# Performance work log

Hardware: AMD Instinct MI355X
Metric: run time of the kernel (lower is better)

## Reference

```python
import jax, jax.numpy as jnp
import numpy as np
from jax import lax

REPR, ACT, HID = 256, 2, 512
BN_EPS = 1e-5


def setup_inputs() -> dict:
    key = jax.random.key(0)
    ks = jax.random.split(key, 12)
    B, H, W, Tm1 = 512, 64, 64, 16
    d_in = REPR + ACT
    s = lambda k, shape, scale: jax.random.normal(k, shape, dtype=jnp.float32) * scale
    return {
        "init_state": jax.random.normal(ks[0], (B, 2, H, W), dtype=jnp.float32),
        "actions": jax.random.normal(ks[1], (B, Tm1, ACT), dtype=jnp.float32),
        "conv_w": s(ks[2], (16, 2, 3, 3), (1.0 / np.sqrt(2 * 9))),
        "bn_gamma": jnp.ones((16,), jnp.float32),
        "bn_beta": jnp.zeros((16,), jnp.float32),
        "enc_fc_w": s(ks[3], (REPR, 16), (1.0 / np.sqrt(16))),
        "enc_fc_b": s(ks[4], (REPR,), 0.01),
        "gru_w_ih": s(ks[5], (3 * HID, d_in), (1.0 / np.sqrt(HID))),
        "gru_w_hh": s(ks[6], (3 * HID, HID), (1.0 / np.sqrt(HID))),
        "gru_b_ih": s(ks[7], (3 * HID,), (1.0 / np.sqrt(HID))),
        "gru_b_hh": s(ks[8], (3 * HID,), (1.0 / np.sqrt(HID))),
        "pred_fc_w": s(ks[9], (REPR, HID), (1.0 / np.sqrt(HID))),
        "pred_fc_b": s(ks[10], (REPR,), 0.01),
    }


def _encoder(x, conv_w, bn_gamma, bn_beta, enc_fc_w, enc_fc_b):
    # Conv2d(2->16, 3x3, stride 1, pad 1, no bias), NCHW
    y = lax.conv_general_dilated(x, conv_w, (1, 1), "SAME",
                                 dimension_numbers=("NCHW", "OIHW", "NCHW"))
    # BatchNorm2d in training mode: batch statistics over (N, H, W)
    mean = jnp.mean(y, axis=(0, 2, 3), keepdims=True)
    var = jnp.var(y, axis=(0, 2, 3), keepdims=True)
    y = (y - mean) * lax.rsqrt(var + BN_EPS)
    y = y * bn_gamma[None, :, None, None] + bn_beta[None, :, None, None]
    y = jax.nn.relu(y)
    # MaxPool2d(2, 2)
    y = lax.reduce_window(y, -jnp.inf, lax.max, (1, 1, 2, 2), (1, 1, 2, 2), "VALID")
    # AdaptiveAvgPool2d((1,1)) + flatten
    y = jnp.mean(y, axis=(2, 3))  # (B, 16)
    return y @ enc_fc_w.T + enc_fc_b  # (B, repr_dim)


def reference(init_state, actions, conv_w, bn_gamma, bn_beta, enc_fc_w, enc_fc_b,
              gru_w_ih, gru_w_hh, gru_b_ih, gru_b_hh, pred_fc_w, pred_fc_b):
    B = init_state.shape[0]
    s0 = _encoder(init_state, conv_w, bn_gamma, bn_beta, enc_fc_w, enc_fc_b)  # (B, R)

    def step(carry, u_t):
        s_prev, h = carry
        x = jnp.concatenate([s_prev, u_t], axis=-1)          # (B, R+A)
        gx = x @ gru_w_ih.T + gru_b_ih                        # (B, 3H)
        gh = h @ gru_w_hh.T + gru_b_hh                        # (B, 3H)
        gx_r, gx_z, gx_n = jnp.split(gx, 3, axis=-1)
        gh_r, gh_z, gh_n = jnp.split(gh, 3, axis=-1)
        r = jax.nn.sigmoid(gx_r + gh_r)
        z = jax.nn.sigmoid(gx_z + gh_z)
        n = jnp.tanh(gx_n + r * gh_n)
        h_new = (1.0 - z) * n + z * h
        s_pred = jax.nn.relu(h_new @ pred_fc_w.T + pred_fc_b)  # (B, R)
        return (s_pred, h_new), s_pred

    h0 = jnp.zeros((B, HID), dtype=s0.dtype)
    u_seq = jnp.transpose(actions, (1, 0, 2))  # (T-1, B, A)
    _, preds = lax.scan(step, (s0, h0), u_seq)  # preds: (T-1, B, R)
    pred_encs = jnp.concatenate([s0[None], preds], axis=0)  # (T, B, R)
    return jnp.transpose(pred_encs, (1, 0, 2))  # (B, T, R)
```

## Files before the change

kernel.cpp:

```cpp
#include <hip/hip_runtime.h>
#include <hip/hip_bf16.h>
#include <math.h>

#define TM1 16
#define TT 17

typedef __attribute__((ext_vector_type(8))) __bf16 bf16x8;
typedef __attribute__((ext_vector_type(4))) float f32x4;

#define OFF_BSTATS 0
#define OFF_STATS  65536
#define OFF_POOLED 65568
#define OFF_BCOL   98336
#define OFF_SPB    104480
#define OFF_PWB    170016
#define OFF_WIHB   235552
#define OFF_WHHB   432160
#define OFF_HB     825376

#define IMG_STRIDE 67
#define SLAB_ROWS 18
#define IMG_CI (SLAB_ROWS * IMG_STRIDE)

__device__ __forceinline__ void stage_slab_bf16(__hip_bfloat16* __restrict__ imgp,
                                                const float* __restrict__ xb, int slab,
                                                int tid) {
  for (int i = tid; i < 2 * SLAB_ROWS * 66; i += 256) {
    const int ci = i / (SLAB_ROWS * 66);
    const int rem = i - ci * (SLAB_ROWS * 66);
    const int lr = rem / 66, c = rem - lr * 66;
    const int gr = slab * 16 - 1 + lr;
    float v = 0.0f;
    if (gr >= 0 && gr < 64 && c >= 1 && c <= 64) v = xb[ci * 4096 + gr * 64 + (c - 1)];
    imgp[ci * IMG_CI + lr * IMG_STRIDE + c] = __float2bfloat16(v);
  }
}

__device__ __forceinline__ void make_k_offsets(int hi, int* off, int* val) {
#pragma unroll
  for (int j = 0; j < 8; ++j) {
    const int k = hi * 8 + j;
    if (k < 18) {
      const int ci = k / 9, r9 = k - ci * 9;
      const int dy = r9 / 3, dx = r9 - dy * 3;
      off[j] = ci * IMG_CI + dy * IMG_STRIDE + dx;
      val[j] = 1;
    } else {
      off[j] = 0;
      val[j] = 0;
    }
  }
}

__device__ __forceinline__ bf16x8 make_conv_bfrag(const float* __restrict__ cw,
                                                  int l15, int hi) {
  __hip_bfloat16 btmp[8];
#pragma unroll
  for (int j = 0; j < 8; ++j) {
    const int k = hi * 8 + j;
    btmp[j] = __float2bfloat16((k < 18) ? cw[l15 * 18 + k] : 0.0f);
  }
  return *(bf16x8*)btmp;
}

__device__ __forceinline__ bf16x8 make_conv_afrag(const __hip_bfloat16* __restrict__ imgp,
                                                  int yloc, int x0, int l15,
                                                  const int* off, const int* val) {
  const int base = yloc * IMG_STRIDE + x0 + l15;
  const __hip_bfloat16 z = __float2bfloat16(0.0f);
  __hip_bfloat16 atmp[8];
#pragma unroll
  for (int j = 0; j < 8; ++j) atmp[j] = val[j] ? imgp[base + off[j]] : z;
  return *(bf16x8*)atmp;
}

__global__ __launch_bounds__(256) void enc_stats_prep(
    const float* __restrict__ x, const float* __restrict__ cw,
    float* __restrict__ bstats,
    const float* __restrict__ wih, const float* __restrict__ whh,
    const float* __restrict__ pw,
    const float* __restrict__ bih, const float* __restrict__ bhh,
    __hip_bfloat16* __restrict__ wihb, __hip_bfloat16* __restrict__ whhb,
    __hip_bfloat16* __restrict__ pwb, float* __restrict__ bcol) {
  {
    const int n1 = 1536 * 256, n2 = 1536 * 512, n3 = 256 * 512, n4 = 512 * 12;
    int i = blockIdx.x * 256 + threadIdx.x;
    int st = gridDim.x * 256;
    for (int j = i; j < n1 + n2 + n3 + n4; j += st) {
      if (j < n1) {
        int r = j >> 8, c = j & 255;
        wihb[j] = __float2bfloat16(wih[r * 258 + c]);
      } else if (j < n1 + n2) {
        int k = j - n1;
        whhb[k] = __float2bfloat16(whh[k]);
      } else if (j < n1 + n2 + n3) {
        int k = j - n1 - n2;
        pwb[k] = __float2bfloat16(pw[k]);
      } else {
        int k = j - n1 - n2 - n3;
        int col = k / 12, e = k - col * 12;
        float v = 0.0f;
        switch (e) {
          case 0: v = bih[col] + bhh[col]; break;
          case 1: v = bih[512 + col] + bhh[512 + col]; break;
          case 2: v = bih[1024 + col]; break;
          case 3: v = bhh[1024 + col]; break;
          case 4: v = wih[col * 258 + 256]; break;
          case 5: v = wih[col * 258 + 257]; break;
          case 6: v = wih[(512 + col) * 258 + 256]; break;
          case 7: v = wih[(512 + col) * 258 + 257]; break;
          case 8: v = wih[(1024 + col) * 258 + 256]; break;
          case 9: v = wih[(1024 + col) * 258 + 257]; break;
          default: v = 0.0f; break;
        }
        bcol[k] = v;
      }
    }
  }

  __shared__ __hip_bfloat16 imgp[2 * IMG_CI];
  __shared__ float redS[4][16], redQ[4][16];
  const int tid = threadIdx.x;
  const int b = blockIdx.x >> 2, slab = blockIdx.x & 3;
  const int wv = tid >> 6, lane = tid & 63;
  const int l15 = lane & 15, hi = lane >> 4;
  stage_slab_bf16(imgp, x + b * 8192, slab, tid);

  int off[8], val[8];
  make_k_offsets(hi, off, val);
  const bf16x8 bfrag = make_conv_bfrag(cw, l15, hi);
  __syncthreads();

  float sacc = 0.0f, qacc = 0.0f;
  const f32x4 zero4 = {0.f, 0.f, 0.f, 0.f};
#pragma unroll
  for (int tp = 0; tp < 8; ++tp) {
    const int tpi = wv * 8 + tp;
    const int y0 = (tpi >> 2) * 2, x0 = (tpi & 3) * 16;
    bf16x8 a0 = make_conv_afrag(imgp, y0, x0, l15, off, val);
    bf16x8 a1 = make_conv_afrag(imgp, y0 + 1, x0, l15, off, val);
    f32x4 c0 = __builtin_amdgcn_mfma_f32_16x16x32_bf16(a0, bfrag, zero4, 0, 0, 0);
    f32x4 c1 = __builtin_amdgcn_mfma_f32_16x16x32_bf16(a1, bfrag, zero4, 0, 0, 0);
#pragma unroll
    for (int i = 0; i < 4; ++i) {
      sacc += c0[i] + c1[i];
      qacc = fmaf(c0[i], c0[i], qacc);
      qacc = fmaf(c1[i], c1[i], qacc);
    }
  }
  sacc += __shfl_down(sacc, 16); sacc += __shfl_down(sacc, 32);
  qacc += __shfl_down(qacc, 16); qacc += __shfl_down(qacc, 32);
  if (lane < 16) { redS[wv][l15] = sacc; redQ[wv][l15] = qacc; }
  __syncthreads();
  if (tid < 16)
    bstats[tid * 2048 + blockIdx.x] =
        redS[0][tid] + redS[1][tid] + redS[2][tid] + redS[3][tid];
  else if (tid < 32) {
    int c = tid - 16;
    bstats[tid * 2048 + blockIdx.x] =
        redQ[0][c] + redQ[1][c] + redQ[2][c] + redQ[3][c];
  }
}

__global__ __launch_bounds__(256) void reduce_stats_k(const float* __restrict__ bstats,
                                                      float* __restrict__ stats) {
  __shared__ float acc[4];
  const int c = blockIdx.x, tid = threadIdx.x;
  const float4 v4 = *(const float4*)(bstats + c * 2048 + tid * 8);
  const float4 w4 = *(const float4*)(bstats + c * 2048 + tid * 8 + 4);
  float v = v4.x + v4.y + v4.z + v4.w + w4.x + w4.y + w4.z + w4.w;
#pragma unroll
  for (int off = 32; off >= 1; off >>= 1) v += __shfl_down(v, off);
  if ((tid & 63) == 0) acc[tid >> 6] = v;
  __syncthreads();
  if (tid == 0) stats[c] = acc[0] + acc[1] + acc[2] + acc[3];
}

__global__ __launch_bounds__(256) void enc_pool(const float* __restrict__ x,
                                                const float* __restrict__ cw,
                                                const float* __restrict__ stats,
                                                const float* __restrict__ gamma,
                                                const float* __restrict__ beta,
                                                float* __restrict__ pooledG) {
  __shared__ __hip_bfloat16 imgp[2 * IMG_CI];
  __shared__ float red[4][16];
  __shared__ float statsL[32];
  const int tid = threadIdx.x;
  const int b = blockIdx.x >> 2, slab = blockIdx.x & 3;
  const int wv = tid >> 6, lane = tid & 63;
  const int l15 = lane & 15, hi = lane >> 4;
  stage_slab_bf16(imgp, x + b * 8192, slab, tid);
  if (tid < 32) statsL[tid] = stats[tid];

  int off[8], val[8];
  make_k_offsets(hi, off, val);
  const bf16x8 bfrag = make_conv_bfrag(cw, l15, hi);
  __syncthreads();

  const float invN = 1.0f / (512.0f * 4096.0f);
  const float m = statsL[l15] * invN;
  const float var = statsL[16 + l15] * invN - m * m;
  const float isd = rsqrtf(var + 1e-5f);
  const float scv = gamma[l15] * isd;
  const float shv = beta[l15] - m * scv;

  float psum = 0.0f;
  const f32x4 zero4 = {0.f, 0.f, 0.f, 0.f};
#pragma unroll
  for (int tp = 0; tp < 8; ++tp) {
    const int tpi = wv * 8 + tp;
    const int y0 = (tpi >> 2) * 2, x0 = (tpi & 3) * 16;
    bf16x8 a0 = make_conv_afrag(imgp, y0, x0, l15, off, val);
    bf16x8 a1 = make_conv_afrag(imgp, y0 + 1, x0, l15, off, val);
    f32x4 c0 = __builtin_amdgcn_mfma_f32_16x16x32_bf16(a0, bfrag, zero4, 0, 0, 0);
    f32x4 c1 = __builtin_amdgcn_mfma_f32_16x16x32_bf16(a1, bfrag, zero4, 0, 0, 0);
#pragma unroll
    for (int p = 0; p < 2; ++p) {
      const float v00 = fmaxf(fmaf(c0[2 * p + 0], scv, shv), 0.0f);
      const float v01 = fmaxf(fmaf(c0[2 * p + 1], scv, shv), 0.0f);
      const float v10 = fmaxf(fmaf(c1[2 * p + 0], scv, shv), 0.0f);
      const float v11 = fmaxf(fmaf(c1[2 * p + 1], scv, shv), 0.0f);
      psum += fmaxf(fmaxf(v00, v01), fmaxf(v10, v11));
    }
  }
  psum += __shfl_down(psum, 16);
  psum += __shfl_down(psum, 32);
  if (lane < 16) red[wv][l15] = psum;
  __syncthreads();
  if (tid < 16)
    pooledG[blockIdx.x * 16 + tid] = red[0][tid] + red[1][tid] + red[2][tid] + red[3][tid];
}

__global__ __launch_bounds__(384) void gru_v2(
    const __hip_bfloat16* __restrict__ spb,
    const __hip_bfloat16* __restrict__ hb_in,
    __hip_bfloat16* __restrict__ hb_out,
    const __hip_bfloat16* __restrict__ wihb,
    const __hip_bfloat16* __restrict__ whhb,
    const float* __restrict__ bcol,
    const float* __restrict__ actions,
    const float* __restrict__ pooledG,
    const float* __restrict__ fcw,
    const float* __restrict__ fcb,
    float* __restrict__ out,
    int t) {
  __shared__ __hip_bfloat16 sF[8 * 64 * 8];
  __shared__ __hip_bfloat16 hF[16 * 64 * 8];
  __shared__ float accL[4][2][256];
  const int tid = threadIdx.x;
  const int w = tid / 64, lane = tid & 63;
  const int l15 = lane & 15, hi = lane >> 4;
  const int cg = blockIdx.x, band = blockIdx.y;
  const int row0 = band * 16;
  const int ct = w & 1, g = w >> 1;

  if (t == 0) {
    float* avgF = &accL[0][0][0];
    if (tid < 256) {
      const int r = tid >> 4, k = tid & 15;
      const int img = row0 + r;
      const float v = pooledG[(img * 4 + 0) * 16 + k] + pooledG[(img * 4 + 1) * 16 + k] +
                      pooledG[(img * 4 + 2) * 16 + k] + pooledG[(img * 4 + 3) * 16 + k];
      avgF[r * 16 + k] = v * (1.0f / 1024.0f);
    }
    __syncthreads();
    for (int i = tid; i < 4096; i += 384) {
      const int kk = i >> 9, rem = i & 511, ln = rem >> 3, e = rem & 7;
      const int r = ln & 15;
      const int col = kk * 32 + (ln >> 4) * 8 + e;
      float v = fcb[col];
#pragma unroll
      for (int k = 0; k < 16; ++k) v = fmaf(avgF[r * 16 + k], fcw[col * 16 + k], v);
      sF[i] = __float2bfloat16(v);
      if (cg == 0) out[((size_t)(row0 + r) * TT + 0) * 256 + col] = v;
    }
  } else {
    for (int i = tid; i < 512; i += 384) {
      int kk = i >> 6, ln = i & 63;
      *(bf16x8*)(sF + i * 8) =
          *(const bf16x8*)(spb + (row0 + (ln & 15)) * 256 + kk * 32 + (ln >> 4) * 8);
    }
    for (int i = tid; i < 1024; i += 384) {
      int kk = i >> 6, ln = i & 63;
      *(bf16x8*)(hF + i * 8) =
          *(const bf16x8*)(hb_in + (row0 + (ln & 15)) * 512 + kk * 32 + (ln >> 4) * 8);
    }
  }
  __syncthreads();

  const int cj = cg * 32 + ct * 16;
  f32x4 accS = {0.f, 0.f, 0.f, 0.f}, accH = accS;
  {
    const __hip_bfloat16* B = wihb + (g * 512 + cj + l15) * 256 + hi * 8;
#pragma unroll
    for (int kk = 0; kk < 8; ++kk) {
      bf16x8 a = *(const bf16x8*)(sF + (kk * 64 + lane) * 8);
      accS = __builtin_amdgcn_mfma_f32_16x16x32_bf16(a, *(const bf16x8*)(B + kk * 32),
                                                     accS, 0, 0, 0);
    }
  }
  if (t > 0) {
    const __hip_bfloat16* B = whhb + (g * 512 + cj + l15) * 512 + hi * 8;
#pragma unroll
    for (int kk = 0; kk < 16; ++kk) {
      bf16x8 a = *(const bf16x8*)(hF + (kk * 64 + lane) * 8);
      accH = __builtin_amdgcn_mfma_f32_16x16x32_bf16(a, *(const bf16x8*)(B + kk * 32),
                                                     accH, 0, 0, 0);
    }
  }
  __syncthreads();
  if (g < 2) {
#pragma unroll
    for (int i = 0; i < 4; ++i)
      accL[g][ct][(hi * 4 + i) * 16 + l15] = accS[i] + accH[i];
  } else {
#pragma unroll
    for (int i = 0; i < 4; ++i) {
      accL[2][ct][(hi * 4 + i) * 16 + l15] = accS[i];
      accL[3][ct][(hi * 4 + i) * 16 + l15] = accH[i];
    }
  }
  __syncthreads();

  if (w < 2) {
    f32x4 vR = *(const f32x4*)&accL[0][w][lane * 4];
    f32x4 vZ = *(const f32x4*)&accL[1][w][lane * 4];
    f32x4 vXN = *(const f32x4*)&accL[2][w][lane * 4];
    f32x4 vHN = *(const f32x4*)&accL[3][w][lane * 4];
    const int r = lane >> 2;
    const int row = row0 + r;
    const float u0 = actions[row * 32 + t * 2 + 0];
    const float u1 = actions[row * 32 + t * 2 + 1];
#pragma unroll
    for (int j = 0; j < 4; ++j) {
      const int c = (lane & 3) * 4 + j;
      const int col = cg * 32 + w * 16 + c;
      const float4 b0 = *(const float4*)(bcol + col * 12);
      const float4 b1 = *(const float4*)(bcol + col * 12 + 4);
      const float4 b2 = *(const float4*)(bcol + col * 12 + 8);
      const float gr = vR[j] + b0.x + u0 * b1.x + u1 * b1.y;
      const float gz = vZ[j] + b0.y + u0 * b1.z + u1 * b1.w;
      const float gxn = vXN[j] + b0.z + u0 * b2.x + u1 * b2.y;
      const float ghn = vHN[j] + b0.w;
      const float rg = 1.0f / (1.0f + __expf(-gr));
      const float zg = 1.0f / (1.0f + __expf(-gz));
      float xn = gxn + rg * ghn;
      xn = fminf(fmaxf(xn, -15.0f), 15.0f);
      const float e = __expf(2.0f * xn);
      const float ng = (e - 1.0f) / (e + 1.0f);
      const float hp = (t > 0) ? (float)hb_in[row * 512 + col] : 0.0f;
      const float hnv = (1.0f - zg) * ng + zg * hp;
      hb_out[row * 512 + col] = __float2bfloat16(hnv);
    }
  }
}

__global__ __launch_bounds__(256) void pred_v2(
    const __hip_bfloat16* __restrict__ hb,
    const __hip_bfloat16* __restrict__ pwb,
    const float* __restrict__ pb,
    float* __restrict__ out,
    __hip_bfloat16* __restrict__ spb,
    int slot) {
  __shared__ float accL[4][256];
  const int tid = threadIdx.x;
  const int w = tid >> 6, lane = tid & 63;
  const int l15 = lane & 15, hi = lane >> 4;
  const int pcg = blockIdx.x, band = blockIdx.y;
  const int row0 = band * 16, pc0 = pcg * 16;
  f32x4 acc = {0.f, 0.f, 0.f, 0.f};
  const __hip_bfloat16* A = hb + (row0 + l15) * 512 + w * 128 + hi * 8;
  const __hip_bfloat16* B = pwb + (pc0 + l15) * 512 + w * 128 + hi * 8;
#pragma unroll
  for (int kk = 0; kk < 4; ++kk)
    acc = __builtin_amdgcn_mfma_f32_16x16x32_bf16(*(const bf16x8*)(A + kk * 32),
                                                  *(const bf16x8*)(B + kk * 32),
                                                  acc, 0, 0, 0);
#pragma unroll
  for (int i = 0; i < 4; ++i) accL[w][(hi * 4 + i) * 16 + l15] = acc[i];
  __syncthreads();
  if (w == 0) {
    f32x4 p0 = *(const f32x4*)&accL[0][lane * 4];
    f32x4 p1 = *(const f32x4*)&accL[1][lane * 4];
    f32x4 p2 = *(const f32x4*)&accL[2][lane * 4];
    f32x4 p3 = *(const f32x4*)&accL[3][lane * 4];
    const int r = lane >> 2;
    const int row = row0 + r;
    float4 ov;
    float* po = &ov.x;
#pragma unroll
    for (int j = 0; j < 4; ++j) {
      const int c = (lane & 3) * 4 + j;
      const int col = pc0 + c;
      float v = p0[j] + p1[j] + p2[j] + p3[j] + pb[col];
      v = fmaxf(v, 0.0f);
      po[j] = v;
      spb[row * 256 + col] = __float2bfloat16(v);
    }
    *(float4*)(out + ((size_t)row * TT + slot) * 256 + pc0 + (lane & 3) * 4) = ov;
  }
}

extern "C" void kernel_launch(void* const* d_in, const int* in_sizes, int n_in,
                              void* d_out, int out_size, void* d_ws, size_t ws_size,
                              hipStream_t stream) {
  const float* x       = (const float*)d_in[0];
  const float* actions = (const float*)d_in[1];
  const float* cw      = (const float*)d_in[2];
  const float* gamma   = (const float*)d_in[3];
  const float* beta    = (const float*)d_in[4];
  const float* fcw     = (const float*)d_in[5];
  const float* fcb     = (const float*)d_in[6];
  const float* wih     = (const float*)d_in[7];
  const float* whh     = (const float*)d_in[8];
  const float* bih     = (const float*)d_in[9];
  const float* bhh     = (const float*)d_in[10];
  const float* pw      = (const float*)d_in[11];
  const float* pb      = (const float*)d_in[12];
  float* out = (float*)d_out;
  float* ws  = (float*)d_ws;

  float* bstats  = ws + OFF_BSTATS;
  float* stats   = ws + OFF_STATS;
  float* pooledG = ws + OFF_POOLED;
  float* bcol    = ws + OFF_BCOL;
  __hip_bfloat16* spb  = (__hip_bfloat16*)(ws + OFF_SPB);
  __hip_bfloat16* pwb  = (__hip_bfloat16*)(ws + OFF_PWB);
  __hip_bfloat16* wihb = (__hip_bfloat16*)(ws + OFF_WIHB);
  __hip_bfloat16* whhb = (__hip_bfloat16*)(ws + OFF_WHHB);
  __hip_bfloat16* hb0  = (__hip_bfloat16*)(ws + OFF_HB);
  __hip_bfloat16* hb1  = hb0 + 512 * 512;

  enc_stats_prep<<<dim3(2048), dim3(256), 0, stream>>>(x, cw, bstats, wih, whh, pw,
                                                       bih, bhh, wihb, whhb, pwb, bcol);
  reduce_stats_k<<<dim3(32), dim3(256), 0, stream>>>(bstats, stats);
  enc_pool<<<dim3(2048), dim3(256), 0, stream>>>(x, cw, stats, gamma, beta, pooledG);
  for (int t = 0; t < TM1; ++t) {
    __hip_bfloat16* hbi = (t & 1) ? hb1 : hb0;
    __hip_bfloat16* hbo = (t & 1) ? hb0 : hb1;
    gru_v2<<<dim3(16, 32), dim3(384), 0, stream>>>(spb, hbi, hbo, wihb, whhb,
                                                   bcol, actions, pooledG, fcw, fcb,
                                                   out, t);
    pred_v2<<<dim3(16, 32), dim3(256), 0, stream>>>(hbo, pwb, pb, out, spb, t + 1);
  }
}
```

Measured before the change: 335.6 us.

## Fuse prediction FC into next GRU step kernel, recomputing per block

Merges the per-step prediction linear layer into the following GRU step kernel. Each block recomputes the 16-row s_pred tile (relu(h @ pred_w^T + b)) from the previous hidden state in shared memory instead of reading it from a separate kernel's output. This halves the kernel launches per timestep and removes the spb global round-trip. The grid shrinks to 8 column groups of 64 columns each, and one trailing pred kernel handles the last output. The cost is redundant pred GEMM work, repeated in each of the 8 column-group blocks, and fewer blocks per launch.

Measured after the change: 379.2 us. +13.0%, slower.

```diff
diff --git a/kernel.cpp b/kernel.cpp
--- a/kernel.cpp
+++ b/kernel.cpp
@@ -231,12 +231,13 @@
     pooledG[blockIdx.x * 16 + tid] = red[0][tid] + red[1][tid] + red[2][tid] + red[3][tid];
 }
 
-__global__ __launch_bounds__(384) void gru_v2(
-    const __hip_bfloat16* __restrict__ spb,
+__global__ __launch_bounds__(384) void fused_step(
     const __hip_bfloat16* __restrict__ hb_in,
     __hip_bfloat16* __restrict__ hb_out,
     const __hip_bfloat16* __restrict__ wihb,
     const __hip_bfloat16* __restrict__ whhb,
+    const __hip_bfloat16* __restrict__ pwb,
+    const float* __restrict__ pb,
     const float* __restrict__ bcol,
     const float* __restrict__ actions,
     const float* __restrict__ pooledG,
@@ -244,17 +245,41 @@
     const float* __restrict__ fcb,
     float* __restrict__ out,
     int t) {
-  __shared__ __hip_bfloat16 sF[8 * 64 * 8];
   __shared__ __hip_bfloat16 hF[16 * 64 * 8];
-  __shared__ float accL[4][2][256];
+  __shared__ __hip_bfloat16 sL[16 * 264];
+  __shared__ float accL[4][4][256];
   const int tid = threadIdx.x;
   const int w = tid / 64, lane = tid & 63;
   const int l15 = lane & 15, hi = lane >> 4;
   const int cg = blockIdx.x, band = blockIdx.y;
   const int row0 = band * 16;
-  const int ct = w & 1, g = w >> 1;
-
-  if (t == 0) {
+
+  if (t > 0) {
+    for (int i = tid; i < 1024; i += 384) {
+      int kk = i >> 6, ln = i & 63;
+      *(bf16x8*)(hF + i * 8) =
+          *(const bf16x8*)(hb_in + (row0 + (ln & 15)) * 512 + kk * 32 + (ln >> 4) * 8);
+    }
+    __syncthreads();
+    for (int ct = w; ct < 16; ct += 6) {
+      const int pc = ct * 16 + l15;
+      const __hip_bfloat16* bp = pwb + (size_t)pc * 512 + hi * 8;
+      f32x4 acc = {0.f, 0.f, 0.f, 0.f};
+#pragma unroll
+      for (int kk = 0; kk < 16; ++kk)
+        acc = __builtin_amdgcn_mfma_f32_16x16x32_bf16(
+            *(const bf16x8*)(hF + (kk * 64 + lane) * 8),
+            *(const bf16x8*)(bp + kk * 32), acc, 0, 0, 0);
+      const float bias = pb[pc];
+#pragma unroll
+      for (int i = 0; i < 4; ++i) {
+        const int r = hi * 4 + i;
+        const float v = fmaxf(acc[i] + bias, 0.0f);
+        sL[r * 264 + pc] = __float2bfloat16(v);
+        if (cg == 0) out[((size_t)(row0 + r) * TT + t) * 256 + pc] = v;
+      }
+    }
+  } else {
     float* avgF = &accL[0][0][0];
     if (tid < 256) {
       const int r = tid >> 4, k = tid & 15;
@@ -265,64 +290,55 @@
     }
     __syncthreads();
     for (int i = tid; i < 4096; i += 384) {
-      const int kk = i >> 9, rem = i & 511, ln = rem >> 3, e = rem & 7;
-      const int r = ln & 15;
-      const int col = kk * 32 + (ln >> 4) * 8 + e;
+      const int r = i >> 8, col = i & 255;
       float v = fcb[col];
 #pragma unroll
       for (int k = 0; k < 16; ++k) v = fmaf(avgF[r * 16 + k], fcw[col * 16 + k], v);
-      sF[i] = __float2bfloat16(v);
+      sL[r * 264 + col] = __float2bfloat16(v);
       if (cg == 0) out[((size_t)(row0 + r) * TT + 0) * 256 + col] = v;
     }
-  } else {
-    for (int i = tid; i < 512; i += 384) {
-      int kk = i >> 6, ln = i & 63;
-      *(bf16x8*)(sF + i * 8) =
-          *(const bf16x8*)(spb + (row0 + (ln & 15)) * 256 + kk * 32 + (ln >> 4) * 8);
-    }
-    for (int i = tid; i < 1024; i += 384) {
-      int kk = i >> 6, ln = i & 63;
-      *(bf16x8*)(hF + i * 8) =
-          *(const bf16x8*)(hb_in + (row0 + (ln & 15)) * 512 + kk * 32 + (ln >> 4) * 8);
-    }
-  }
-  __syncthreads();
-
-  const int cj = cg * 32 + ct * 16;
-  f32x4 accS = {0.f, 0.f, 0.f, 0.f}, accH = accS;
-  {
-    const __hip_bfloat16* B = wihb + (g * 512 + cj + l15) * 256 + hi * 8;
-#pragma unroll
-    for (int kk = 0; kk < 8; ++kk) {
-      bf16x8 a = *(const bf16x8*)(sF + (kk * 64 + lane) * 8);
-      accS = __builtin_amdgcn_mfma_f32_16x16x32_bf16(a, *(const bf16x8*)(B + kk * 32),
-                                                     accS, 0, 0, 0);
-    }
-  }
-  if (t > 0) {
-    const __hip_bfloat16* B = whhb + (g * 512 + cj + l15) * 512 + hi * 8;
-#pragma unroll
-    for (int kk = 0; kk < 16; ++kk) {
-      bf16x8 a = *(const bf16x8*)(hF + (kk * 64 + lane) * 8);
-      accH = __builtin_amdgcn_mfma_f32_16x16x32_bf16(a, *(const bf16x8*)(B + kk * 32),
-                                                     accH, 0, 0, 0);
-    }
-  }
-  __syncthreads();
-  if (g < 2) {
-#pragma unroll
-    for (int i = 0; i < 4; ++i)
-      accL[g][ct][(hi * 4 + i) * 16 + l15] = accS[i] + accH[i];
-  } else {
-#pragma unroll
-    for (int i = 0; i < 4; ++i) {
-      accL[2][ct][(hi * 4 + i) * 16 + l15] = accS[i];
-      accL[3][ct][(hi * 4 + i) * 16 + l15] = accH[i];
-    }
-  }
-  __syncthreads();
-
-  if (w < 2) {
+  }
+  __syncthreads();
+
+#pragma unroll
+  for (int jj = 0; jj < 2; ++jj) {
+    const int job = 2 * w + jj;
+    const int g = job >> 2, ct4 = job & 3;
+    const int jb = cg * 64 + ct4 * 16 + l15;
+    f32x4 accS = {0.f, 0.f, 0.f, 0.f}, accH = accS;
+    {
+      const __hip_bfloat16* B = wihb + (size_t)(g * 512 + jb) * 256 + hi * 8;
+#pragma unroll
+      for (int kk = 0; kk < 8; ++kk) {
+        bf16x8 a = *(const bf16x8*)&sL[l15 * 264 + kk * 32 + hi * 8];
+        accS = __builtin_amdgcn_mfma_f32_16x16x32_bf16(a, *(const bf16x8*)(B + kk * 32),
+                                                       accS, 0, 0, 0);
+      }
+    }
+    if (t > 0) {
+      const __hip_bfloat16* B = whhb + (size_t)(g * 512 + jb) * 512 + hi * 8;
+#pragma unroll
+      for (int kk = 0; kk < 16; ++kk) {
+        bf16x8 a = *(const bf16x8*)(hF + (kk * 64 + lane) * 8);
+        accH = __builtin_amdgcn_mfma_f32_16x16x32_bf16(a, *(const bf16x8*)(B + kk * 32),
+                                                       accH, 0, 0, 0);
+      }
+    }
+    if (g < 2) {
+#pragma unroll
+      for (int i = 0; i < 4; ++i)
+        accL[g][ct4][(hi * 4 + i) * 16 + l15] = accS[i] + accH[i];
+    } else {
+#pragma unroll
+      for (int i = 0; i < 4; ++i) {
+        accL[2][ct4][(hi * 4 + i) * 16 + l15] = accS[i];
+        accL[3][ct4][(hi * 4 + i) * 16 + l15] = accH[i];
+      }
+    }
+  }
+  __syncthreads();
+
+  if (w < 4) {
     f32x4 vR = *(const f32x4*)&accL[0][w][lane * 4];
     f32x4 vZ = *(const f32x4*)&accL[1][w][lane * 4];
     f32x4 vXN = *(const f32x4*)&accL[2][w][lane * 4];
@@ -334,7 +350,7 @@
 #pragma unroll
     for (int j = 0; j < 4; ++j) {
       const int c = (lane & 3) * 4 + j;
-      const int col = cg * 32 + w * 16 + c;
+      const int col = cg * 64 + w * 16 + c;
       const float4 b0 = *(const float4*)(bcol + col * 12);
       const float4 b1 = *(const float4*)(bcol + col * 12 + 4);
       const float4 b2 = *(const float4*)(bcol + col * 12 + 8);
@@ -438,9 +454,8 @@
   for (int t = 0; t < TM1; ++t) {
     __hip_bfloat16* hbi = (t & 1) ? hb1 : hb0;
     __hip_bfloat16* hbo = (t & 1) ? hb0 : hb1;
-    gru_v2<<<dim3(16, 32), dim3(384), 0, stream>>>(spb, hbi, hbo, wihb, whhb,
-                                                   bcol, actions, pooledG, fcw, fcb,
-                                                   out, t);
-    pred_v2<<<dim3(16, 32), dim3(256), 0, stream>>>(hbo, pwb, pb, out, spb, t + 1);
-  }
-}
+    fused_step<<<dim3(8, 32), dim3(384), 0, stream>>>(
+        hbi, hbo, wihb, whhb, pwb, pb, bcol, actions, pooledG, fcw, fcb, out, t);
+  }
+  pred_v2<<<dim3(16, 32), dim3(256), 0, stream>>>(hb0, pwb, pb, out, spb, 16);
+}
```
